# Kernel optimization log

Hardware: AMD Instinct MI355X
Metric: run time of the kernel (lower is better)

The kernel has to match this reference:

```python
import jax, jax.numpy as jnp
import numpy as np

# init kwargs (constants)
MIN_ = 1      # bg samples
MAX_ = 1      # fg samples
KSZ = 3       # dilation kernel size
IGNORE = -255 # seg_ignore_idx
EPS = 1e-6

B, H, W = 128, 512, 512


def setup_inputs() -> dict:
    key = jax.random.key(0)
    k1, k2, k3 = jax.random.split(key, 3)
    x = jax.random.uniform(k1, (B, 1, H, W), dtype=jnp.float32)   # CAM, nonneg
    u_fg = jax.random.uniform(k2, (B, H * W), dtype=jnp.float32)  # noise for fg multinomial
    u_bg = jax.random.uniform(k3, (B, H * W), dtype=jnp.float32)  # noise for bg multinomial
    return {"x": x, "u_fg": u_fg, "u_bg": u_bg}


def _sample_mask(logw, u, k):
    """Weighted sampling without replacement via Gumbel-top-k (== torch.multinomial).
    logw: [B, HW] log-weights; u: [B, HW] uniform noise. Returns binary [B, HW] int32 mask."""
    g = -jnp.log(-jnp.log(jnp.clip(u, 1e-12, 1.0 - 1e-12)))
    idx = jax.lax.top_k(logw + g, k)[1]  # [B, k]
    mask = jnp.zeros(logw.shape, dtype=jnp.int32)
    return mask.at[jnp.arange(logw.shape[0])[:, None], idx].set(1)


def _dilate(m):
    """Morphological dilation of binary mask [B,H,W] with KSZ x KSZ ones structuring element
    == max-pool with SAME padding."""
    if KSZ == 1:
        return m
    return jax.lax.reduce_window(m, jnp.int32(0), jax.lax.max,
                                 (1, KSZ, KSZ), (1, 1, 1), 'SAME')


def reference(x, u_fg, u_bg):
    b, _, h, w = x.shape
    cam = x[:, 0].reshape(b, h * w)
    p = cam + EPS
    p = p / p.sum(axis=1, keepdims=True)           # normalized CAM (fg weights)
    fg = _sample_mask(jnp.log(p), u_fg, MAX_).reshape(b, h, w)
    bg = _sample_mask(jnp.log1p(-p), u_bg, MIN_).reshape(b, h, w)  # bg weights = 1 - p
    fg = _dilate(fg)
    bg = _dilate(bg)
    overlap = (fg + bg) == 2
    fg = jnp.where(overlap, 0, fg)
    bg = jnp.where(overlap, 0, bg)
    out = jnp.full((b, h, w), IGNORE, dtype=jnp.int32)
    out = jnp.where(fg == 1, 1, out)
    out = jnp.where(bg == 1, 0, out)  # bg written last, as in torch
    return out
```

## Files before the change

### kernel.cpp

```cpp
#include <hip/hip_runtime.h>

#define NB 128
#define HH 512
#define WW 512
#define HW (HH * WW)

constexpr float EPS_F = 1e-6f;
constexpr int IGNORE_V = -255;

constexpr int BPR = 32;
constexpr int TPB = 256;
constexpr int EPB = HW / BPR;
constexpr int F4_PER_THREAD = EPB / (TPB * 4);

__global__ __launch_bounds__(TPB) void k_sum_fill(const float* __restrict__ cam,
                                                  int* __restrict__ out,
                                                  float* __restrict__ partial) {
    const int b = blockIdx.y;
    const int chunk = blockIdx.x;
    const long base = (long)b * HW + (long)chunk * EPB;
    const float4* c4 = (const float4*)(cam + base);
    int4* o4 = (int4*)(out + base);
    const int t = threadIdx.x;
    const int4 fill = make_int4(IGNORE_V, IGNORE_V, IGNORE_V, IGNORE_V);

    float s = 0.f;
#pragma unroll
    for (int i = 0; i < F4_PER_THREAD; ++i) {
        float4 v = c4[t + i * TPB];
        s += (v.x + EPS_F) + (v.y + EPS_F) + (v.z + EPS_F) + (v.w + EPS_F);
        o4[t + i * TPB] = fill;
    }
#pragma unroll
    for (int off = 32; off > 0; off >>= 1) s += __shfl_down(s, off, 64);
    __shared__ float ls[TPB / 64];
    if ((t & 63) == 0) ls[t >> 6] = s;
    __syncthreads();
    if (t == 0) {
        float tot = 0.f;
#pragma unroll
        for (int w = 0; w < TPB / 64; ++w) tot += ls[w];
        partial[b * BPR + chunk] = tot;
    }
}

__device__ inline unsigned long long pack_key(float f, unsigned idx) {
    unsigned bits = __float_as_uint(f);
    bits ^= (bits & 0x80000000u) ? 0xFFFFFFFFu : 0x80000000u;
    return ((unsigned long long)bits << 32) | (unsigned)(~idx);
}

__global__ __launch_bounds__(TPB) void k_argmax(const float* __restrict__ cam,
                                                const float* __restrict__ ufg,
                                                const float* __restrict__ ubg,
                                                const float* __restrict__ partial,
                                                unsigned long long* __restrict__ bestFg,
                                                unsigned long long* __restrict__ bestBg) {
    const int b = blockIdx.y;
    const int chunk = blockIdx.x;
    const int t = threadIdx.x;

    float S = 0.f;
    for (int i = 0; i < BPR; ++i) S += partial[b * BPR + i];

    const long base = (long)b * HW + (long)chunk * EPB;
    const float4* c4 = (const float4*)(cam + base);
    const float4* f4 = (const float4*)(ufg + base);
    const float4* g4 = (const float4*)(ubg + base);

    unsigned long long bf = 0ull, bb = 0ull;
#pragma unroll
    for (int i = 0; i < F4_PER_THREAD; ++i) {
        float4 v = c4[t + i * TPB];
        float4 uf = f4[t + i * TPB];
        float4 ub = g4[t + i * TPB];
        const unsigned idx0 = (unsigned)(chunk * EPB) + (unsigned)((t + i * TPB) * 4);
        float vv[4] = {v.x, v.y, v.z, v.w};
        float uu[4] = {uf.x, uf.y, uf.z, uf.w};
        float wwn[4] = {ub.x, ub.y, ub.z, ub.w};
#pragma unroll
        for (int j = 0; j < 4; ++j) {
            float p = (vv[j] + EPS_F) / S;
            float gf = -logf(-logf(fmaxf(uu[j], 1e-12f)));
            float wf = logf(p) + gf;
            float gb = -logf(-logf(fmaxf(wwn[j], 1e-12f)));
            float wb = log1pf(-p) + gb;
            unsigned long long kf = pack_key(wf, idx0 + j);
            unsigned long long kb = pack_key(wb, idx0 + j);
            bf = kf > bf ? kf : bf;
            bb = kb > bb ? kb : bb;
        }
    }
#pragma unroll
    for (int off = 32; off > 0; off >>= 1) {
        unsigned long long of = __shfl_down(bf, off, 64);
        unsigned long long ob = __shfl_down(bb, off, 64);
        bf = of > bf ? of : bf;
        bb = ob > bb ? ob : bb;
    }
    __shared__ unsigned long long lf[TPB / 64], lb[TPB / 64];
    if ((t & 63) == 0) { lf[t >> 6] = bf; lb[t >> 6] = bb; }
    __syncthreads();
    if (t == 0) {
        for (int w = 1; w < TPB / 64; ++w) {
            if (lf[w] > bf) bf = lf[w];
            if (lb[w] > bb) bb = lb[w];
        }
        bestFg[b * BPR + chunk] = bf;
        bestBg[b * BPR + chunk] = bb;
    }
}

__global__ void k_fixup(const unsigned long long* __restrict__ bestFg,
                        const unsigned long long* __restrict__ bestBg,
                        int* __restrict__ out) {
    const int b = threadIdx.x;
    if (b >= NB) return;
    unsigned long long bf = 0ull, bb = 0ull;
    for (int i = 0; i < BPR; ++i) {
        unsigned long long f = bestFg[b * BPR + i];
        unsigned long long g = bestBg[b * BPR + i];
        if (f > bf) bf = f;
        if (g > bb) bb = g;
    }
    const unsigned fidx = ~(unsigned)(bf & 0xFFFFFFFFull);
    const unsigned bidx = ~(unsigned)(bb & 0xFFFFFFFFull);
    const int fr = (int)(fidx / WW), fc = (int)(fidx % WW);
    const int br = (int)(bidx / WW), bc = (int)(bidx % WW);
    const long rb = (long)b * HW;

    for (int dr = -1; dr <= 1; ++dr) {
        for (int dc = -1; dc <= 1; ++dc) {
            int r = fr + dr, c = fc + dc;
            if (r >= 0 && r < HH && c >= 0 && c < WW) {
                bool inBg = (r >= br - 1 && r <= br + 1 && c >= bc - 1 && c <= bc + 1);
                if (!inBg) out[rb + (long)r * WW + c] = 1;
            }
            r = br + dr; c = bc + dc;
            if (r >= 0 && r < HH && c >= 0 && c < WW) {
                bool inFg = (r >= fr - 1 && r <= fr + 1 && c >= fc - 1 && c <= fc + 1);
                if (!inFg) out[rb + (long)r * WW + c] = 0;
            }
        }
    }
}

extern "C" void kernel_launch(void* const* d_in, const int* in_sizes, int n_in,
                              void* d_out, int out_size, void* d_ws, size_t ws_size,
                              hipStream_t stream) {
    const float* cam = (const float*)d_in[0];
    const float* ufg = (const float*)d_in[1];
    const float* ubg = (const float*)d_in[2];
    int* out = (int*)d_out;

    float* partial = (float*)d_ws;
    unsigned long long* bestFg = (unsigned long long*)((char*)d_ws + 16384);
    unsigned long long* bestBg = (unsigned long long*)((char*)d_ws + 49152);

    dim3 grid(BPR, NB);
    k_sum_fill<<<grid, TPB, 0, stream>>>(cam, out, partial);
    k_argmax<<<grid, TPB, 0, stream>>>(cam, ufg, ubg, partial, bestFg, bestBg);
    k_fixup<<<1, 128, 0, stream>>>(bestFg, bestBg, out);
}
```

Before: 489.6 us.

## Move fg argmax into sum pass and use ratio form of Gumbel keys

The foreground Gumbel-max no longer depends on the normalized probability, so it is computed in the first pass alongside the sum and fill, using the monotone equivalent key a/E with E = -log(u). The background key similarly becomes (S - a)/E, which removes log, log1p and the double log per element. The second pass now reads only cam and u_bg instead of cam, u_fg and u_bg, cutting both memory traffic and transcendental work. The risk is slight tie and rounding differences versus the log-space keys, for example from dropping the upper clamp on u, which could select a different index in rare cases.

```diff
diff --git a/kernel.cpp b/kernel.cpp
--- a/kernel.cpp
+++ b/kernel.cpp
@@ -13,49 +13,71 @@
 constexpr int EPB = HW / BPR;
 constexpr int F4_PER_THREAD = EPB / (TPB * 4);
 
-__global__ __launch_bounds__(TPB) void k_sum_fill(const float* __restrict__ cam,
-                                                  int* __restrict__ out,
-                                                  float* __restrict__ partial) {
-    const int b = blockIdx.y;
-    const int chunk = blockIdx.x;
-    const long base = (long)b * HW + (long)chunk * EPB;
-    const float4* c4 = (const float4*)(cam + base);
-    int4* o4 = (int4*)(out + base);
-    const int t = threadIdx.x;
-    const int4 fill = make_int4(IGNORE_V, IGNORE_V, IGNORE_V, IGNORE_V);
-
-    float s = 0.f;
-#pragma unroll
-    for (int i = 0; i < F4_PER_THREAD; ++i) {
-        float4 v = c4[t + i * TPB];
-        s += (v.x + EPS_F) + (v.y + EPS_F) + (v.z + EPS_F) + (v.w + EPS_F);
-        o4[t + i * TPB] = fill;
-    }
-#pragma unroll
-    for (int off = 32; off > 0; off >>= 1) s += __shfl_down(s, off, 64);
-    __shared__ float ls[TPB / 64];
-    if ((t & 63) == 0) ls[t >> 6] = s;
-    __syncthreads();
-    if (t == 0) {
-        float tot = 0.f;
-#pragma unroll
-        for (int w = 0; w < TPB / 64; ++w) tot += ls[w];
-        partial[b * BPR + chunk] = tot;
-    }
-}
-
 __device__ inline unsigned long long pack_key(float f, unsigned idx) {
     unsigned bits = __float_as_uint(f);
     bits ^= (bits & 0x80000000u) ? 0xFFFFFFFFu : 0x80000000u;
     return ((unsigned long long)bits << 32) | (unsigned)(~idx);
 }
 
-__global__ __launch_bounds__(TPB) void k_argmax(const float* __restrict__ cam,
-                                                const float* __restrict__ ufg,
-                                                const float* __restrict__ ubg,
-                                                const float* __restrict__ partial,
-                                                unsigned long long* __restrict__ bestFg,
-                                                unsigned long long* __restrict__ bestBg) {
+__global__ __launch_bounds__(TPB) void k_fg_sum_fill(const float* __restrict__ cam,
+                                                     const float* __restrict__ ufg,
+                                                     int* __restrict__ out,
+                                                     float* __restrict__ partial,
+                                                     unsigned long long* __restrict__ bestFg) {
+    const int b = blockIdx.y;
+    const int chunk = blockIdx.x;
+    const long base = (long)b * HW + (long)chunk * EPB;
+    const float4* c4 = (const float4*)(cam + base);
+    const float4* f4 = (const float4*)(ufg + base);
+    int4* o4 = (int4*)(out + base);
+    const int t = threadIdx.x;
+    const int4 fill = make_int4(IGNORE_V, IGNORE_V, IGNORE_V, IGNORE_V);
+
+    float s = 0.f;
+    unsigned long long bf = 0ull;
+#pragma unroll
+    for (int i = 0; i < F4_PER_THREAD; ++i) {
+        float4 v = c4[t + i * TPB];
+        float4 uf = f4[t + i * TPB];
+        o4[t + i * TPB] = fill;
+        const unsigned idx0 = (unsigned)(chunk * EPB) + (unsigned)((t + i * TPB) * 4);
+        float vv[4] = {v.x, v.y, v.z, v.w};
+        float uu[4] = {uf.x, uf.y, uf.z, uf.w};
+#pragma unroll
+        for (int j = 0; j < 4; ++j) {
+            float a = vv[j] + EPS_F;
+            s += a;
+            float E = -logf(fmaxf(uu[j], 1e-12f));
+            unsigned long long kf = pack_key(a / E, idx0 + j);
+            bf = kf > bf ? kf : bf;
+        }
+    }
+#pragma unroll
+    for (int off = 32; off > 0; off >>= 1) {
+        s += __shfl_down(s, off, 64);
+        unsigned long long of = __shfl_down(bf, off, 64);
+        bf = of > bf ? of : bf;
+    }
+    __shared__ float ls[TPB / 64];
+    __shared__ unsigned long long lf[TPB / 64];
+    if ((t & 63) == 0) { ls[t >> 6] = s; lf[t >> 6] = bf; }
+    __syncthreads();
+    if (t == 0) {
+        float tot = 0.f;
+#pragma unroll
+        for (int w = 0; w < TPB / 64; ++w) {
+            tot += ls[w];
+            if (lf[w] > bf) bf = lf[w];
+        }
+        partial[b * BPR + chunk] = tot;
+        bestFg[b * BPR + chunk] = bf;
+    }
+}
+
+__global__ __launch_bounds__(TPB) void k_bg(const float* __restrict__ cam,
+                                            const float* __restrict__ ubg,
+                                            const float* __restrict__ partial,
+                                            unsigned long long* __restrict__ bestBg) {
     const int b = blockIdx.y;
     const int chunk = blockIdx.x;
     const int t = threadIdx.x;
@@ -65,48 +87,35 @@
 
     const long base = (long)b * HW + (long)chunk * EPB;
     const float4* c4 = (const float4*)(cam + base);
-    const float4* f4 = (const float4*)(ufg + base);
     const float4* g4 = (const float4*)(ubg + base);
 
-    unsigned long long bf = 0ull, bb = 0ull;
+    unsigned long long bb = 0ull;
 #pragma unroll
     for (int i = 0; i < F4_PER_THREAD; ++i) {
         float4 v = c4[t + i * TPB];
-        float4 uf = f4[t + i * TPB];
         float4 ub = g4[t + i * TPB];
         const unsigned idx0 = (unsigned)(chunk * EPB) + (unsigned)((t + i * TPB) * 4);
         float vv[4] = {v.x, v.y, v.z, v.w};
-        float uu[4] = {uf.x, uf.y, uf.z, uf.w};
-        float wwn[4] = {ub.x, ub.y, ub.z, ub.w};
+        float uu[4] = {ub.x, ub.y, ub.z, ub.w};
 #pragma unroll
         for (int j = 0; j < 4; ++j) {
-            float p = (vv[j] + EPS_F) / S;
-            float gf = -logf(-logf(fmaxf(uu[j], 1e-12f)));
-            float wf = logf(p) + gf;
-            float gb = -logf(-logf(fmaxf(wwn[j], 1e-12f)));
-            float wb = log1pf(-p) + gb;
-            unsigned long long kf = pack_key(wf, idx0 + j);
-            unsigned long long kb = pack_key(wb, idx0 + j);
-            bf = kf > bf ? kf : bf;
+            float num = S - (vv[j] + EPS_F);
+            float E = -logf(fmaxf(uu[j], 1e-12f));
+            unsigned long long kb = pack_key(num / E, idx0 + j);
             bb = kb > bb ? kb : bb;
         }
     }
 #pragma unroll
     for (int off = 32; off > 0; off >>= 1) {
-        unsigned long long of = __shfl_down(bf, off, 64);
         unsigned long long ob = __shfl_down(bb, off, 64);
-        bf = of > bf ? of : bf;
         bb = ob > bb ? ob : bb;
     }
-    __shared__ unsigned long long lf[TPB / 64], lb[TPB / 64];
-    if ((t & 63) == 0) { lf[t >> 6] = bf; lb[t >> 6] = bb; }
+    __shared__ unsigned long long lb[TPB / 64];
+    if ((t & 63) == 0) lb[t >> 6] = bb;
     __syncthreads();
     if (t == 0) {
-        for (int w = 1; w < TPB / 64; ++w) {
-            if (lf[w] > bf) bf = lf[w];
+        for (int w = 1; w < TPB / 64; ++w)
             if (lb[w] > bb) bb = lb[w];
-        }
-        bestFg[b * BPR + chunk] = bf;
         bestBg[b * BPR + chunk] = bb;
     }
 }
@@ -158,7 +167,7 @@
     unsigned long long* bestBg = (unsigned long long*)((char*)d_ws + 49152);
 
     dim3 grid(BPR, NB);
-    k_sum_fill<<<grid, TPB, 0, stream>>>(cam, out, partial);
-    k_argmax<<<grid, TPB, 0, stream>>>(cam, ufg, ubg, partial, bestFg, bestBg);
+    k_fg_sum_fill<<<grid, TPB, 0, stream>>>(cam, ufg, out, partial, bestFg);
+    k_bg<<<grid, TPB, 0, stream>>>(cam, ubg, partial, bestBg);
     k_fixup<<<1, 128, 0, stream>>>(bestFg, bestBg, out);
 }
```

New measurement: 426.9 us. -12.8%, faster.
